# Kernel optimization log

Measured on AMD Instinct MI355X. Metric: run time of the kernel, lower is better.

The kernel has to match this reference:

```python
import jax, jax.numpy as jnp
import numpy as np

SR = 44100        # sample rate (init arg)
WIN = 442         # FFT window length from tensor[i:i+442]
HOP = 4           # loop stride
NBINS = 221       # kept spectrum bins x[:221]
THR = 0.01        # threshold passed to inner fftLayer
REL = 0.0594      # relative pitch-change threshold
BIN_HZ = 100.0    # argmax*100 -> frequency


def _windows_and_mag(tensor):
    n = tensor.shape[0]
    n_win = (n - WIN + HOP - 1) // HOP
    starts = jnp.arange(n_win) * HOP
    windows = tensor[starts[:, None] + jnp.arange(WIN)[None, :]]
    spec = jnp.fft.fft(windows, axis=-1)[:, :NBINS]           # complex64 [n_win, 221]
    spec = jnp.where(jnp.abs(spec) < THR, jnp.zeros_like(spec), spec)  # fftLayer threshold
    mag = jnp.abs(spec.real) + jnp.abs(spec.imag)             # |re| + |im|, as in forward
    return mag, starts


def setup_inputs() -> dict:
    key = jax.random.key(0)
    return {"tensor": jax.random.normal(key, (1_000_000,), dtype=jnp.float32)}


def reference(tensor):
    mag, starts = _windows_and_mag(tensor)
    # per-window dominant frequency: argmax bin * 100 Hz
    tmp = jnp.argmax(mag, axis=-1).astype(jnp.float32) * BIN_HZ    # [n_win]
    i_samp = starts.astype(jnp.float32)                            # sample index of each window

    def step(carry, x):
        maxF, Ftime = carry
        t, i = x
        cond = jnp.abs(maxF - t) > maxF * REL
        emit_f = maxF
        emit_d = (i - Ftime) * 1000.0 / SR
        maxF = jnp.where(cond, t, maxF)
        Ftime = jnp.where(cond, i, Ftime)
        return (maxF, Ftime), (cond, emit_f, emit_d)

    (maxF, Ftime), (flags, freqs, durs) = jax.lax.scan(
        step, (jnp.float32(0.0), jnp.float32(0.0)), (tmp, i_samp))
    # trailing append after the loop: (maxF, (i_last - Ftime)*1000/44100)
    final = jnp.stack([maxF, (i_samp[-1] - Ftime) * 1000.0 / SR])
    # flags marks windows where a note boundary was emitted; (freqs, durs) at those
    # positions are the (maxF, duration_ms) pairs the original appends to `out`.
    return flags, freqs, durs, final
```

## Files before the change

### kernel.cpp

```cpp
#include <hip/hip_runtime.h>

#define WIN 442
#define HOP 4
#define NBINS 221
#define LC 64
#define SPAN 704
#define B2 1024
#define NG 32

constexpr double kPI = 3.14159265358979323846264338327950288;

constexpr double tsin_poly(double r) {
    double t = r, s = r;
    for (int n = 1; n <= 9; ++n) { t *= -(r * r) / ((2.0 * n) * (2.0 * n + 1.0)); s += t; }
    return s;
}
constexpr double tcos_poly(double r) {
    double t = 1.0, c = 1.0;
    for (int n = 1; n <= 9; ++n) { t *= -(r * r) / ((2.0 * n - 1.0) * (2.0 * n)); c += t; }
    return c;
}
struct SC { double s, c; };
constexpr SC tsincos(double a) {
    int q = (int)(a / (kPI / 2) + 0.5);
    double r = a - q * (kPI / 2);
    double sr = tsin_poly(r), cr = tcos_poly(r);
    switch (q & 3) {
        case 0: return {sr, cr};
        case 1: return {cr, -sr};
        case 2: return {-sr, -cr};
        default: return {-cr, sr};
    }
}
struct TabF { float c[WIN]; float s[WIN]; };
constexpr TabF make_tabf() {
    TabF t{};
    for (int i = 0; i < WIN; ++i) {
        SC sc = tsincos(2.0 * kPI * (double)i / 442.0);
        t.c[i] = (float)sc.c; t.s[i] = (float)(-sc.s);
    }
    return t;
}
struct TabR { double c4[NBINS], s4[NBINS], c8[NBINS], s8[NBINS]; };
constexpr TabR make_tabr() {
    TabR t{};
    for (int k = 0; k < NBINS; ++k) {
        SC a = tsincos(2.0 * kPI * (double)((4 * k) % WIN) / 442.0);
        t.c4[k] = a.c; t.s4[k] = a.s;
        SC b = tsincos(2.0 * kPI * (double)((8 * k) % WIN) / 442.0);
        t.c8[k] = b.c; t.s8[k] = b.s;
    }
    return t;
}
__constant__ TabF cTabF = make_tabf();
__constant__ TabR cTabR = make_tabr();

static __device__ __forceinline__ unsigned long long shflx64(unsigned long long v, int off) {
    unsigned int lo = (unsigned int)v, hi = (unsigned int)(v >> 32);
    lo = __shfl_xor(lo, off, 64);
    hi = __shfl_xor(hi, off, 64);
    return ((unsigned long long)hi << 32) | lo;
}

__global__ __launch_bounds__(128) void k_slide(
    const float* __restrict__ x, int n, int n_win, int n_chunks,
    int* __restrict__ a_arr) {
    __shared__ __align__(16) float Xs[SPAN];
    __shared__ __align__(16) float Ds_[LC * 4];
    __shared__ unsigned long long cand[LC][9];

    const int tid = threadIdx.x;
    const int lane = tid & 63;
    const int wc = tid >> 6;
    const int chunk = blockIdx.x;
    const int s0 = chunk * (LC * HOP);

    for (int i = tid; i < SPAN; i += 128) {
        int g = s0 + i;
        Xs[i] = (g < n) ? x[g] : 0.0f;
    }
    __syncthreads();
    for (int r = tid; r < LC * 4; r += 128) Ds_[r] = Xs[r + WIN] - Xs[r];
    __syncthreads();

    const int wlen = min(LC, n_win - chunk * LC);

    const int k0 = lane + 128 * wc, k1 = k0 + 64;
    const bool a0 = (k0 < NBINS), a1 = (k1 < NBINS);
    const int kk0 = a0 ? k0 : 0, kk1 = a1 ? k1 : 0;
    const unsigned int lo0 = 255u - (unsigned)k0, lo1 = 255u - (unsigned)k1;

    float ec0[8], es0[8], ec1[8], es1[8];
    {
        int t0 = 0, t1 = 0;
#pragma unroll
        for (int m = 1; m < 8; ++m) {
            t0 += kk0; if (t0 >= WIN) t0 -= WIN;
            ec0[m] = cTabF.c[t0]; es0[m] = cTabF.s[t0];
            t1 += kk1; if (t1 >= WIN) t1 -= WIN;
            ec1[m] = cTabF.c[t1]; es1[m] = cTabF.s[t1];
        }
    }
    double C40 = a0 ? cTabR.c4[kk0] : 0.0, S40 = a0 ? cTabR.s4[kk0] : 0.0;
    double C41 = a1 ? cTabR.c4[kk1] : 0.0, S41 = a1 ? cTabR.s4[kk1] : 0.0;
    const double C80 = cTabR.c8[kk0], S80 = cTabR.s8[kk0];
    const double C81 = cTabR.c8[kk1], S81 = cTabR.s8[kk1];

    double S0r, S0i, S1r, S1i;
    {
        float xa = Xs[440], xb = Xs[441];
        S0r = (double)fmaf(xb, ec0[1], xa);
        S0i = (double)(xb * es0[1]);
        S1r = (double)fmaf(xb, ec1[1], xa);
        S1i = (double)(xb * es1[1]);
        const float4* Xq = (const float4*)Xs;
#pragma unroll 1
        for (int t = 54; t >= 0; --t) {
            float4 va = Xq[2 * t], vb = Xq[2 * t + 1];
            float Dr0 = va.x;
            Dr0 = fmaf(va.y, ec0[1], Dr0); Dr0 = fmaf(va.z, ec0[2], Dr0);
            Dr0 = fmaf(va.w, ec0[3], Dr0); Dr0 = fmaf(vb.x, ec0[4], Dr0);
            Dr0 = fmaf(vb.y, ec0[5], Dr0); Dr0 = fmaf(vb.z, ec0[6], Dr0);
            Dr0 = fmaf(vb.w, ec0[7], Dr0);
            float Di0 = va.y * es0[1];
            Di0 = fmaf(va.z, es0[2], Di0); Di0 = fmaf(va.w, es0[3], Di0);
            Di0 = fmaf(vb.x, es0[4], Di0); Di0 = fmaf(vb.y, es0[5], Di0);
            Di0 = fmaf(vb.z, es0[6], Di0); Di0 = fmaf(vb.w, es0[7], Di0);
            double nr = fma(S0r, C80, fma(S0i, S80, (double)Dr0));
            double ni = fma(S0i, C80, fma(S0r, -S80, (double)Di0));
            S0r = nr; S0i = ni;
            float Dr1 = va.x;
            Dr1 = fmaf(va.y, ec1[1], Dr1); Dr1 = fmaf(va.z, ec1[2], Dr1);
            Dr1 = fmaf(va.w, ec1[3], Dr1); Dr1 = fmaf(vb.x, ec1[4], Dr1);
            Dr1 = fmaf(vb.y, ec1[5], Dr1); Dr1 = fmaf(vb.z, ec1[6], Dr1);
            Dr1 = fmaf(vb.w, ec1[7], Dr1);
            float Di1 = va.y * es1[1];
            Di1 = fmaf(va.z, es1[2], Di1); Di1 = fmaf(va.w, es1[3], Di1);
            Di1 = fmaf(vb.x, es1[4], Di1); Di1 = fmaf(vb.y, es1[5], Di1);
            Di1 = fmaf(vb.z, es1[6], Di1); Di1 = fmaf(vb.w, es1[7], Di1);
            nr = fma(S1r, C81, fma(S1i, S81, (double)Dr1));
            ni = fma(S1i, C81, fma(S1r, -S81, (double)Di1));
            S1r = nr; S1i = ni;
        }
    }
    if (!a0) { S0r = 0.0; S0i = 0.0; }
    if (!a1) { S1r = 0.0; S1i = 0.0; }

    const float4* Dq = (const float4*)Ds_;
    for (int b = 0; b < 8; ++b) {
        unsigned long long key[8];
#pragma unroll
        for (int u = 0; u < 8; ++u) {
            if (b | u) {
                float4 d = Dq[b * 8 + u - 1];
                float Dr0 = fmaf(d.w, ec0[3], fmaf(d.z, ec0[2], fmaf(d.y, ec0[1], d.x)));
                float Di0 = fmaf(d.w, es0[3], fmaf(d.z, es0[2], d.y * es0[1]));
                double nr = S0r + (double)Dr0;
                double ni = S0i + (double)Di0;
                S0r = fma(nr, C40, -(ni * S40));
                S0i = fma(nr, S40, ni * C40);
                float Dr1 = fmaf(d.w, ec1[3], fmaf(d.z, ec1[2], fmaf(d.y, ec1[1], d.x)));
                float Di1 = fmaf(d.w, es1[3], fmaf(d.z, es1[2], d.y * es1[1]));
                nr = S1r + (double)Dr1;
                ni = S1i + (double)Di1;
                S1r = fma(nr, C41, -(ni * S41));
                S1i = fma(nr, S41, ni * C41);
            }
            float m0 = (float)(fabs(S0r) + fabs(S0i));
            float m1 = (float)(fabs(S1r) + fabs(S1i));
            unsigned long long key0 = ((unsigned long long)__float_as_uint(m0) << 32) | lo0;
            unsigned long long key1 = ((unsigned long long)__float_as_uint(m1) << 32) | lo1;
            key[u] = (key1 > key0) ? key1 : key0;
        }
#pragma unroll
        for (int s = 0; s < 4; ++s) {
            const int off = 32 >> s;
#pragma unroll
            for (int u = 0; u < 8; ++u) {
                unsigned long long o = shflx64(key[u], off);
                if (o > key[u]) key[u] = o;
            }
        }
        if (lane < 4) {
#pragma unroll
            for (int u = 0; u < 8; ++u) cand[b * 8 + u][wc * 4 + lane] = key[u];
        }
    }
    __syncthreads();
    if (tid < wlen) {
        unsigned long long best = cand[tid][0];
#pragma unroll
        for (int i = 1; i < 8; ++i) {
            unsigned long long c = cand[tid][i];
            if (c > best) best = c;
        }
        a_arr[chunk * LC + tid] = 255 - (int)(best & 255u);
    }
}

__global__ __launch_bounds__(256) void k_maps(const int* __restrict__ a_arr, int n_win,
                                              int L2, int* __restrict__ M0) {
    __shared__ float tf[256];
    __shared__ int ti[256];
    int j = blockIdx.x;
    int wbeg = j * L2;
    int cnt = n_win - wbeg; if (cnt > L2) cnt = L2; if (cnt < 0) cnt = 0;
    for (int i = threadIdx.x; i < cnt; i += 256) {
        int a = a_arr[wbeg + i];
        ti[i] = a; tf[i] = 100.0f * (float)a;
    }
    __syncthreads();
    int b = threadIdx.x;
    if (b < NBINS) {
        float mF = 100.0f * (float)b;
        int bin = b, rw = -1;
        for (int i = 0; i < cnt; ++i) {
            float t = tf[i];
            if (fabsf(mF - t) > mF * 0.0594f) { mF = t; bin = ti[i]; rw = wbeg + i; }
        }
        M0[j * NBINS + b] = ((rw + 1) << 8) | bin;
    }
}

__global__ __launch_bounds__(256) void k_sm1(const int* __restrict__ M0,
                                             int* __restrict__ M1) {
    __shared__ int sm[32 * NBINS];
    int g = blockIdx.x;
    for (int i = threadIdx.x; i < 32 * NBINS; i += 256) sm[i] = M0[g * 32 * NBINS + i];
    __syncthreads();
    int b = threadIdx.x;
    if (b < NBINS) {
        int bin = b, rw = -1;
        for (int i = 0; i < 32; ++i) {
            int mp = sm[i * NBINS + bin];
            if (mp >> 8) { rw = (mp >> 8) - 1; bin = mp & 255; }
        }
        M1[g * NBINS + b] = ((rw + 1) << 8) | bin;
    }
}

__global__ __launch_bounds__(256) void k_e0(const int* __restrict__ M0,
                                            const int* __restrict__ M1,
                                            int* __restrict__ E0) {
    __shared__ int sm1[NG * NBINS];
    __shared__ int sm0[32 * NBINS];
    int g = blockIdx.x;
    for (int i = threadIdx.x; i < NG * NBINS; i += 256) sm1[i] = M1[i];
    for (int i = threadIdx.x; i < 32 * NBINS; i += 256) sm0[i] = M0[g * 32 * NBINS + i];
    __syncthreads();
    int j = threadIdx.x;
    if (j < 32) {
        int bin = 0, rw = -1;
        for (int i = 0; i < g; ++i) {
            int mp = sm1[i * NBINS + bin];
            if (mp >> 8) { rw = (mp >> 8) - 1; bin = mp & 255; }
        }
        for (int i = 0; i < j; ++i) {
            int mp = sm0[i * NBINS + bin];
            if (mp >> 8) { rw = (mp >> 8) - 1; bin = mp & 255; }
        }
        E0[g * 32 + j] = ((rw + 1) << 8) | bin;
    }
}

__global__ __launch_bounds__(256) void k_emit(const int* __restrict__ a_arr,
    const int* __restrict__ E0, int n_win, int L2,
    float* __restrict__ flags, float* __restrict__ freqs, float* __restrict__ durs,
    float* __restrict__ out_final) {
    __shared__ float tf[256];
    int j = blockIdx.x;
    int wbeg = j * L2;
    int cnt = n_win - wbeg; if (cnt > L2) cnt = L2;
    if (cnt <= 0) return;
    for (int i = threadIdx.x; i < cnt; i += 256) tf[i] = 100.0f * (float)a_arr[wbeg + i];
    __syncthreads();
    int t = threadIdx.x;
    if (t < cnt) {
        int st = E0[j];
        float maxF = 100.0f * (float)(st & 255);
        int rw = (st >> 8) - 1;
        float Ftime = (rw < 0) ? 0.0f : 4.0f * (float)rw;
        for (int i = 0; i < t; ++i) {
            float tv = tf[i];
            if (fabsf(maxF - tv) > maxF * 0.0594f) {
                maxF = tv; Ftime = 4.0f * (float)(wbeg + i);
            }
        }
        int w = wbeg + t;
        float tv = tf[t];
        float iw = 4.0f * (float)w;
        bool cond = fabsf(maxF - tv) > maxF * 0.0594f;
        flags[w] = cond ? 1.0f : 0.0f;
        freqs[w] = maxF;
        durs[w] = (iw - Ftime) * 1000.0f / 44100.0f;
        if (w == n_win - 1) {
            float fMax = cond ? tv : maxF;
            float fT   = cond ? iw : Ftime;
            out_final[0] = fMax;
            out_final[1] = (iw - fT) * 1000.0f / 44100.0f;
        }
    }
}

extern "C" void kernel_launch(void* const* d_in, const int* in_sizes, int n_in,
                              void* d_out, int out_size, void* d_ws, size_t ws_size,
                              hipStream_t stream) {
    const float* x = (const float*)d_in[0];
    int n = in_sizes[0];
    int n_win = (n - WIN + HOP - 1) / HOP;
    float* out = (float*)d_out;
    char* ws = (char*)d_ws;

    int n_chunks = (n_win + LC - 1) / LC;
    int L2 = (n_win + B2 - 1) / B2;

    int* a_arr = (int*)(ws + 0);
    int* M0    = (int*)(ws + 1000448);
    int* M1    = (int*)(ws + 1905664);
    int* E0    = (int*)(ws + 1933952);

    k_slide<<<dim3(n_chunks), dim3(128), 0, stream>>>(x, n, n_win, n_chunks, a_arr);
    k_maps<<<dim3(B2), dim3(256), 0, stream>>>(a_arr, n_win, L2, M0);
    k_sm1<<<dim3(NG), dim3(256), 0, stream>>>(M0, M1);
    k_e0<<<dim3(NG), dim3(256), 0, stream>>>(M0, M1, E0);
    k_emit<<<dim3(B2), dim3(256), 0, stream>>>(a_arr, E0, n_win, L2,
                                               out, out + (size_t)n_win,
                                               out + 2 * (size_t)n_win,
                                               out + 3 * (size_t)n_win);
}
```

Baseline: 176.6 us.

## Map one bin per thread and double windows per block in sliding DFT

```diff
diff --git a/kernel.cpp b/kernel.cpp
--- a/kernel.cpp
+++ b/kernel.cpp
@@ -3,8 +3,8 @@
 #define WIN 442
 #define HOP 4
 #define NBINS 221
-#define LC 64
-#define SPAN 704
+#define LC 128
+#define SPAN 960
 #define B2 1024
 #define NG 32
 
@@ -62,12 +62,12 @@
     return ((unsigned long long)hi << 32) | lo;
 }
 
-__global__ __launch_bounds__(128) void k_slide(
+__global__ __launch_bounds__(256) void k_slide(
     const float* __restrict__ x, int n, int n_win, int n_chunks,
     int* __restrict__ a_arr) {
     __shared__ __align__(16) float Xs[SPAN];
     __shared__ __align__(16) float Ds_[LC * 4];
-    __shared__ unsigned long long cand[LC][9];
+    __shared__ unsigned long long cand[LC][17];
 
     const int tid = threadIdx.x;
     const int lane = tid & 63;
@@ -75,44 +75,38 @@
     const int chunk = blockIdx.x;
     const int s0 = chunk * (LC * HOP);
 
-    for (int i = tid; i < SPAN; i += 128) {
+    for (int i = tid; i < SPAN; i += 256) {
         int g = s0 + i;
         Xs[i] = (g < n) ? x[g] : 0.0f;
     }
     __syncthreads();
-    for (int r = tid; r < LC * 4; r += 128) Ds_[r] = Xs[r + WIN] - Xs[r];
+    for (int r = tid; r < LC * 4; r += 256) Ds_[r] = Xs[r + WIN] - Xs[r];
     __syncthreads();
 
     const int wlen = min(LC, n_win - chunk * LC);
 
-    const int k0 = lane + 128 * wc, k1 = k0 + 64;
-    const bool a0 = (k0 < NBINS), a1 = (k1 < NBINS);
-    const int kk0 = a0 ? k0 : 0, kk1 = a1 ? k1 : 0;
-    const unsigned int lo0 = 255u - (unsigned)k0, lo1 = 255u - (unsigned)k1;
-
-    float ec0[8], es0[8], ec1[8], es1[8];
+    const int k0 = tid;
+    const bool a0 = (k0 < NBINS);
+    const int kk0 = a0 ? k0 : 0;
+    const unsigned int lo0 = 255u - (unsigned)k0;
+
+    float ec0[8], es0[8];
     {
-        int t0 = 0, t1 = 0;
+        int t0 = 0;
 #pragma unroll
         for (int m = 1; m < 8; ++m) {
             t0 += kk0; if (t0 >= WIN) t0 -= WIN;
             ec0[m] = cTabF.c[t0]; es0[m] = cTabF.s[t0];
-            t1 += kk1; if (t1 >= WIN) t1 -= WIN;
-            ec1[m] = cTabF.c[t1]; es1[m] = cTabF.s[t1];
         }
     }
     double C40 = a0 ? cTabR.c4[kk0] : 0.0, S40 = a0 ? cTabR.s4[kk0] : 0.0;
-    double C41 = a1 ? cTabR.c4[kk1] : 0.0, S41 = a1 ? cTabR.s4[kk1] : 0.0;
     const double C80 = cTabR.c8[kk0], S80 = cTabR.s8[kk0];
-    const double C81 = cTabR.c8[kk1], S81 = cTabR.s8[kk1];
-
-    double S0r, S0i, S1r, S1i;
+
+    double S0r, S0i;
     {
         float xa = Xs[440], xb = Xs[441];
         S0r = (double)fmaf(xb, ec0[1], xa);
         S0i = (double)(xb * es0[1]);
-        S1r = (double)fmaf(xb, ec1[1], xa);
-        S1i = (double)(xb * es1[1]);
         const float4* Xq = (const float4*)Xs;
 #pragma unroll 1
         for (int t = 54; t >= 0; --t) {
@@ -129,25 +123,12 @@
             double nr = fma(S0r, C80, fma(S0i, S80, (double)Dr0));
             double ni = fma(S0i, C80, fma(S0r, -S80, (double)Di0));
             S0r = nr; S0i = ni;
-            float Dr1 = va.x;
-            Dr1 = fmaf(va.y, ec1[1], Dr1); Dr1 = fmaf(va.z, ec1[2], Dr1);
-            Dr1 = fmaf(va.w, ec1[3], Dr1); Dr1 = fmaf(vb.x, ec1[4], Dr1);
-            Dr1 = fmaf(vb.y, ec1[5], Dr1); Dr1 = fmaf(vb.z, ec1[6], Dr1);
-            Dr1 = fmaf(vb.w, ec1[7], Dr1);
-            float Di1 = va.y * es1[1];
-            Di1 = fmaf(va.z, es1[2], Di1); Di1 = fmaf(va.w, es1[3], Di1);
-            Di1 = fmaf(vb.x, es1[4], Di1); Di1 = fmaf(vb.y, es1[5], Di1);
-            Di1 = fmaf(vb.z, es1[6], Di1); Di1 = fmaf(vb.w, es1[7], Di1);
-            nr = fma(S1r, C81, fma(S1i, S81, (double)Dr1));
-            ni = fma(S1i, C81, fma(S1r, -S81, (double)Di1));
-            S1r = nr; S1i = ni;
         }
     }
     if (!a0) { S0r = 0.0; S0i = 0.0; }
-    if (!a1) { S1r = 0.0; S1i = 0.0; }
 
     const float4* Dq = (const float4*)Ds_;
-    for (int b = 0; b < 8; ++b) {
+    for (int b = 0; b < 16; ++b) {
         unsigned long long key[8];
 #pragma unroll
         for (int u = 0; u < 8; ++u) {
@@ -159,18 +140,9 @@
                 double ni = S0i + (double)Di0;
                 S0r = fma(nr, C40, -(ni * S40));
                 S0i = fma(nr, S40, ni * C40);
-                float Dr1 = fmaf(d.w, ec1[3], fmaf(d.z, ec1[2], fmaf(d.y, ec1[1], d.x)));
-                float Di1 = fmaf(d.w, es1[3], fmaf(d.z, es1[2], d.y * es1[1]));
-                nr = S1r + (double)Dr1;
-                ni = S1i + (double)Di1;
-                S1r = fma(nr, C41, -(ni * S41));
-                S1i = fma(nr, S41, ni * C41);
             }
             float m0 = (float)(fabs(S0r) + fabs(S0i));
-            float m1 = (float)(fabs(S1r) + fabs(S1i));
-            unsigned long long key0 = ((unsigned long long)__float_as_uint(m0) << 32) | lo0;
-            unsigned long long key1 = ((unsigned long long)__float_as_uint(m1) << 32) | lo1;
-            key[u] = (key1 > key0) ? key1 : key0;
+            key[u] = ((unsigned long long)__float_as_uint(m0) << 32) | lo0;
         }
 #pragma unroll
         for (int s = 0; s < 4; ++s) {
@@ -190,7 +162,7 @@
     if (tid < wlen) {
         unsigned long long best = cand[tid][0];
 #pragma unroll
-        for (int i = 1; i < 8; ++i) {
+        for (int i = 1; i < 16; ++i) {
             unsigned long long c = cand[tid][i];
             if (c > best) best = c;
         }
@@ -319,7 +291,7 @@
     int* M1    = (int*)(ws + 1905664);
     int* E0    = (int*)(ws + 1933952);
 
-    k_slide<<<dim3(n_chunks), dim3(128), 0, stream>>>(x, n, n_win, n_chunks, a_arr);
+    k_slide<<<dim3(n_chunks), dim3(256), 0, stream>>>(x, n, n_win, n_chunks, a_arr);
     k_maps<<<dim3(B2), dim3(256), 0, stream>>>(a_arr, n_win, L2, M0);
     k_sm1<<<dim3(NG), dim3(256), 0, stream>>>(M0, M1);
     k_e0<<<dim3(NG), dim3(256), 0, stream>>>(M0, M1, E0);
```

Measured after the change: 201.6 us. 1.14x slower.
